# Optimization experiments

Measured on AMD Instinct MI355X. Metric: run time of the kernel, lower is better.

Reference implementation:

```python
import jax, jax.numpy as jnp
import numpy as np

DIM = 512
HEADS = 8
HEAD = DIM // HEADS
T = 243          # temporal length, fixed by get_temporal_mask(243, ...)
N_JOINTS = 17    # skeleton joints
BATCH = 4        # number of clips; leading dim of x is BATCH*T
WINDOWS = (9, 27, 81, 243)  # temporal_MoE_type


def _temporal_masks():
    # Block-diagonal window masks: 0 inside each window block, -100000 outside,
    # exactly matching get_temporal_mask + torch.where(matrix == 0, -100000, 0).
    idx = np.arange(T)
    masks = np.stack([
        np.where((idx[:, None] // w) == (idx[None, :] // w), 0.0, -100000.0)
        for w in WINDOWS
    ]).astype(np.float32)  # (E, T, T)
    return jnp.asarray(masks)


def setup_inputs() -> dict:
    key = jax.random.key(0)
    k0, k1, k2, k3 = jax.random.split(key, 4)
    scaled = lambda k, shape, fan: jax.random.normal(k, shape, jnp.float32) * (fan ** -0.5)
    return {
        "x": jax.random.normal(k0, (BATCH * T, N_JOINTS, DIM), jnp.float32),
        "qkv_w": scaled(k1, (DIM, 3 * DIM), DIM),          # qkv (no bias, qkv_bias=False)
        "proj_w": scaled(k2, (DIM, DIM), DIM),             # output projection
        "proj_b": jnp.zeros((DIM,), jnp.float32),
        "te_w": scaled(k3, (DIM, len(WINDOWS)), DIM),      # temporal_expert_linear
        "te_b": jnp.zeros((len(WINDOWS),), jnp.float32),
        "seqlen": T,
    }


def reference(x, qkv_w, proj_w, proj_b, te_w, te_b, seqlen):
    BT, n, C = x.shape              # (b*T, N, C)
    b = BT // seqlen
    scale = HEAD ** -0.5
    # qkv projection -> q,k,v each (b, H, N, T, head_dim)
    qkv = (x @ qkv_w).reshape(b, seqlen, n, 3, HEADS, HEAD)
    qkv = jnp.transpose(qkv, (3, 0, 4, 2, 1, 5))  # (3, b, H, N, T, c)
    q, k, v = qkv[0], qkv[1], qkv[2]
    # temporal attention logits, shared across experts: (b, H, N, T, T)
    attn = jnp.einsum('bhntc,bhnsc->bhnts', q, k) * scale
    masks = _temporal_masks()                       # (E, T, T)
    attn = attn[None] + masks[:, None, None, None]  # (E, b, H, N, T, T)
    attn = jax.nn.softmax(attn, axis=-1)            # attn_drop is identity (p=0 / eval)
    eo = jnp.einsum('ebhnts,bhnsc->ebhntc', attn, v)
    E = masks.shape[0]
    # (E,b,H,N,T,c) -> (E,b,T,N,H,c) -> (E, b*T, N, C), matching permute(0,3,2,1,4)
    eo = jnp.transpose(eo, (0, 1, 4, 3, 2, 5)).reshape(E, BT, n, C)
    # expert gating: softmax(temporal_expert_linear(x)) over experts, per token
    w = jax.nn.softmax(x @ te_w + te_b, axis=-1)    # (BT, N, E)
    out = jnp.einsum('ebnc,bne->bnc', eo, w)        # fused expert recombination
    out = out @ proj_w + proj_b                     # proj (proj_drop identity)
    return out
```

## Files before the change

kernel.cpp:

```cpp
#include <hip/hip_runtime.h>
#include <hip/hip_bf16.h>
#include <cstdint>

#define TT 243
#define NJ 17
#define NB 4
#define NH 8
#define HD 64
#define CDIM 512
#define NROWS (NB*TT*NJ)
#define NBHN (NB*NH*NJ)

typedef unsigned short u16;
typedef __attribute__((ext_vector_type(8))) short short8;
typedef __attribute__((ext_vector_type(4))) float f32x4;

#define MFMA16(a, b, c) __builtin_amdgcn_mfma_f32_16x16x32_bf16((a), (b), (c), 0, 0, 0)

__device__ __forceinline__ void gl_lds16(const void* g, void* l) {
  __builtin_amdgcn_global_load_lds(
      (const __attribute__((address_space(1))) void*)g,
      (__attribute__((address_space(3))) void*)l, 16, 0, 0);
}

__device__ __forceinline__ u16 f2bf(float f) {
  union { float f; unsigned u; } v; v.f = f;
  unsigned r = v.u + 0x7FFFu + ((v.u >> 16) & 1u);
  return (u16)(r >> 16);
}

__device__ __forceinline__ float wave_reduce_sum(float v) {
#pragma unroll
  for (int off = 32; off > 0; off >>= 1) v += __shfl_xor(v, off, 64);
  return v;
}

__global__ __launch_bounds__(256) void convgates(
    const float* __restrict__ x, const float* __restrict__ te_w,
    const float* __restrict__ te_b, u16* __restrict__ xb,
    float* __restrict__ gates) {
  int w = threadIdx.x >> 6, l = threadIdx.x & 63;
  int row = blockIdx.x * 4 + w;
  if (row >= NROWS) return;
  const float* xr = x + (size_t)row * CDIM;
  u16* xo = xb + (size_t)row * CDIM;
  float a0 = 0.f, a1 = 0.f, a2 = 0.f, a3 = 0.f;
#pragma unroll
  for (int p = 0; p < 2; ++p) {
    int c = (p * 64 + l) * 4;
    float4 v = *(const float4*)(xr + c);
    ushort4 o;
    o.x = f2bf(v.x); o.y = f2bf(v.y); o.z = f2bf(v.z); o.w = f2bf(v.w);
    *(ushort4*)(xo + c) = o;
    float xv[4] = {v.x, v.y, v.z, v.w};
#pragma unroll
    for (int q = 0; q < 4; ++q) {
      float4 wv = *(const float4*)(te_w + (size_t)(c + q) * 4);
      a0 += xv[q] * wv.x; a1 += xv[q] * wv.y;
      a2 += xv[q] * wv.z; a3 += xv[q] * wv.w;
    }
  }
  a0 = wave_reduce_sum(a0);
  a1 = wave_reduce_sum(a1);
  a2 = wave_reduce_sum(a2);
  a3 = wave_reduce_sum(a3);
  a0 += te_b[0]; a1 += te_b[1]; a2 += te_b[2]; a3 += te_b[3];
  float mx = fmaxf(fmaxf(a0, a1), fmaxf(a2, a3));
  float e0 = __expf(a0 - mx), e1 = __expf(a1 - mx);
  float e2 = __expf(a2 - mx), e3 = __expf(a3 - mx);
  float inv = 1.f / (e0 + e1 + e2 + e3);
  if (l == 0) {
    *(float4*)(gates + (size_t)row * 4) =
        make_float4(e0 * inv, e1 * inv, e2 * inv, e3 * inv);
  }
}

__global__ __launch_bounds__(256) void trans_w(const float* __restrict__ in,
                                               u16* __restrict__ out, int K, int N) {
  __shared__ float tile[32][33];
  int n0 = blockIdx.x * 32, k0 = blockIdx.y * 32;
  int tx = threadIdx.x & 31, ty = threadIdx.x >> 5;
#pragma unroll
  for (int p = 0; p < 4; ++p)
    tile[ty + p * 8][tx] = in[(size_t)(k0 + ty + p * 8) * N + n0 + tx];
  __syncthreads();
#pragma unroll
  for (int p = 0; p < 4; ++p)
    out[(size_t)(n0 + ty + p * 8) * K + k0 + tx] = f2bf(tile[tx][ty + p * 8]);
}

__global__ __launch_bounds__(256) void qkv_gemm(
    const u16* __restrict__ xb, const u16* __restrict__ wt,
    u16* __restrict__ qh, u16* __restrict__ kh, u16* __restrict__ vb) {
  __shared__ u16 S[16640];
  u16* Al = S;
  u16* Bl = S + 8192;
  int tid = threadIdx.x;
  int w = tid >> 6, l = tid & 63;
  int c16 = tid & 15, g4 = (tid >> 4) & 3;
  int r0 = blockIdx.x * 128, n0 = blockIdx.y * 128;
  int wm = w & 1, wn = w >> 1;

  size_t arow[2]; int ac8[2], brow[2];
#pragma unroll
  for (int it = 0; it < 2; ++it) {
    int F = it * 256 + w * 64 + l;
    int row = F >> 2;
    ac8[it] = F & 3;
    brow[it] = n0 + row;
    int m = r0 + row; if (m >= NROWS) m = NROWS - 1;
    int bj = m / 243, t = m - bj * 243;
    int b = bj / 17, j = bj - b * 17;
    arow[it] = ((size_t)(b * 243 + t) * 17 + j) * 512;
  }

  f32x4 acc[4][4] = {};
  for (int k0 = 0; k0 < CDIM; k0 += 32) {
    __syncthreads();
#pragma unroll
    for (int it = 0; it < 2; ++it) {
      gl_lds16(xb + arow[it] + k0 + ac8[it] * 8,
               Al + (size_t)(it * 256 + w * 64) * 8);
      gl_lds16(wt + (size_t)brow[it] * 512 + k0 + ac8[it] * 8,
               Bl + (size_t)(it * 256 + w * 64) * 8);
    }
    __syncthreads();
    short8 af[4], bf[4];
#pragma unroll
    for (int i = 0; i < 4; ++i)
      af[i] = *(const short8*)(Al + ((wm * 64 + i * 16 + c16) * 32 + g4 * 8));
#pragma unroll
    for (int j = 0; j < 4; ++j)
      bf[j] = *(const short8*)(Bl + ((wn * 64 + j * 16 + c16) * 32 + g4 * 8));
#pragma unroll
    for (int i = 0; i < 4; ++i)
#pragma unroll
      for (int j = 0; j < 4; ++j)
        acc[i][j] = MFMA16(af[i], bf[j], acc[i][j]);
  }

  if (n0 < 1024) {
#pragma unroll
    for (int i = 0; i < 4; ++i)
#pragma unroll
      for (int r = 0; r < 4; ++r) {
        int m = r0 + wm * 64 + i * 16 + g4 * 4 + r;
        if (m >= NROWS) continue;
        int bj = m / 243, t = m - bj * 243;
        int b = bj / 17, j = bj - b * 17;
#pragma unroll
        for (int jt = 0; jt < 4; ++jt) {
          int col = n0 + wn * 64 + jt * 16 + c16;
          int sel = col >> 9, h = (col >> 6) & 7, c = col & 63;
          u16* dst = sel ? kh : qh;
          dst[((size_t)((b * 8 + h) * 17 + j) * 243 + t) * 64 + c] =
              f2bf(acc[i][jt][r]);
        }
      }
  } else {
    __syncthreads();
#pragma unroll
    for (int i = 0; i < 4; ++i)
#pragma unroll
      for (int jt = 0; jt < 4; ++jt)
#pragma unroll
        for (int r = 0; r < 4; ++r) {
          int row = wm * 64 + i * 16 + g4 * 4 + r;
          int colI = wn * 64 + jt * 16 + c16;
          S[colI * 130 + row] = f2bf(acc[i][jt][r]);
        }
    __syncthreads();
    int hb = (n0 - 1024) >> 6;
    int m0 = r0 + 2 * l;
    int m1 = m0 + 1;
    bool v0 = m0 < NROWS, v1 = m1 < NROWS;
    int bj0 = m0 / 243, t0 = m0 - bj0 * 243;
    int b0 = bj0 / 17, j0 = bj0 - b0 * 17;
    int bj1 = m1 / 243, t1 = m1 - bj1 * 243;
    int b1 = bj1 / 17, j1 = bj1 - b1 * 17;
    size_t base0 = ((size_t)(b0 * 136 + j0) * 64) * 256 + t0;
    size_t base1 = ((size_t)(b1 * 136 + j1) * 64) * 256 + t1;
#pragma unroll 8
    for (int cc = 0; cc < 32; ++cc) {
      int colI = w * 32 + cc;
      int h = hb + (colI >> 6), c = colI & 63;
      ushort2 u = *(const ushort2*)&S[colI * 130 + 2 * l];
      size_t hoff = ((size_t)h * 17 * 64) * 256 + (size_t)c * 256;
      if (v0) vb[base0 + hoff] = u.x;
      if (v1) vb[base1 + hoff] = u.y;
    }
  }
}

__global__ __launch_bounds__(256) void attn_kernel(
    const u16* __restrict__ qh, const u16* __restrict__ kh,
    const u16* __restrict__ vb, const float* __restrict__ gates,
    u16* __restrict__ preb) {
  __shared__ u16 L[32768];
  int bhn = blockIdx.x;
  int q0 = blockIdx.y * 64;
  int b = bhn / (NH * NJ);
  int hj = bhn - b * (NH * NJ);
  int h = hj / NJ, j = hj - (hj / NJ) * NJ;
  int tid = threadIdx.x;
  int w = tid >> 6, l = tid & 63;
  int c16 = tid & 15, g4 = (tid >> 4) & 3;
  int qw = w * 16;

#pragma unroll
  for (int it = 0; it < 8; ++it) {
    int F = it * 256 + w * 64 + l;
    int s = F >> 3;
    int c8 = (F & 7) ^ (s & 7);
    int sg = s < TT ? s : TT - 1;
    gl_lds16(kh + ((size_t)bhn * 243 + sg) * 64 + c8 * 8,
             L + (size_t)(it * 256 + w * 64) * 8);
  }
#pragma unroll
  for (int it = 0; it < 2; ++it) {
    int F = it * 256 + w * 64 + l;
    int q = F >> 3;
    int c8 = (F & 7) ^ (q & 7);
    int t = q0 + q; int tg = t < TT ? t : TT - 1;
    gl_lds16(qh + ((size_t)bhn * 243 + tg) * 64 + c8 * 8,
             L + 16384 + (size_t)(it * 256 + w * 64) * 8);
  }
  __syncthreads();

  short8 aq[2];
#pragma unroll
  for (int hh = 0; hh < 2; ++hh) {
    int q = qw + c16;
    aq[hh] = *(const short8*)(L + 16384 + q * 64 + ((hh * 4 + g4) ^ (q & 7)) * 8);
  }
  f32x4 acc[16];
#pragma unroll
  for (int st = 0; st < 16; ++st) acc[st] = (f32x4)(0.f);
#pragma unroll
  for (int st = 0; st < 16; ++st) {
    int s = st * 16 + c16;
#pragma unroll
    for (int hh = 0; hh < 2; ++hh) {
      short8 bk = *(const short8*)(L + s * 64 + ((hh * 4 + g4) ^ (s & 7)) * 8);
      acc[st] = MFMA16(aq[hh], bk, acc[st]);
    }
  }
  __syncthreads();

#pragma unroll
  for (int it = 0; it < 8; ++it) {
    int F = it * 256 + w * 64 + l;
    int c = F >> 5;
    int slot = F & 31;
    int c8 = (slot & 24) | ((slot & 7) ^ (c & 7));
    gl_lds16(vb + ((size_t)bhn * 64 + c) * 256 + c8 * 8,
             L + 16384 + (size_t)(it * 256 + w * 64) * 8);
  }

  int tr[4], t9[4], t27[4], t81[4];
#pragma unroll
  for (int r = 0; r < 4; ++r) {
    tr[r] = q0 + qw + g4 * 4 + r;
    t9[r] = tr[r] / 9; t27[r] = t9[r] / 3; t81[r] = t27[r] / 3;
  }
#pragma unroll
  for (int st = 0; st < 16; ++st) {
    int s = st * 16 + c16;
#pragma unroll
    for (int r = 0; r < 4; ++r) {
      float v = acc[st][r] * 0.125f;
      acc[st][r] = (s < TT) ? v : -1e30f;
    }
  }
  float M[4];
#pragma unroll
  for (int r = 0; r < 4; ++r) {
    float m = -1e30f;
#pragma unroll
    for (int st = 0; st < 16; ++st) m = fmaxf(m, acc[st][r]);
    m = fmaxf(m, __shfl_xor(m, 1, 64));
    m = fmaxf(m, __shfl_xor(m, 2, 64));
    m = fmaxf(m, __shfl_xor(m, 4, 64));
    m = fmaxf(m, __shfl_xor(m, 8, 64));
    M[r] = m;
  }
#pragma unroll
  for (int st = 0; st < 16; ++st)
#pragma unroll
    for (int r = 0; r < 4; ++r) acc[st][r] = __expf(acc[st][r] - M[r]);
  int s9[16], s27[16], s81[16];
#pragma unroll
  for (int st = 0; st < 16; ++st) {
    int s = st * 16 + c16;
    s9[st] = s / 9; s27[st] = s9[st] / 3; s81[st] = s27[st] / 3;
  }
  float l9[4], l27[4], l81[4], l243[4];
#pragma unroll
  for (int r = 0; r < 4; ++r) { l9[r] = 0.f; l27[r] = 0.f; l81[r] = 0.f; l243[r] = 0.f; }
#pragma unroll
  for (int st = 0; st < 16; ++st)
#pragma unroll
    for (int r = 0; r < 4; ++r) {
      float e = acc[st][r];
      l243[r] += e;
      l9[r]  += (s9[st]  == t9[r])  ? e : 0.f;
      l27[r] += (s27[st] == t27[r]) ? e : 0.f;
      l81[r] += (s81[st] == t81[r]) ? e : 0.f;
    }
#pragma unroll
  for (int r = 0; r < 4; ++r) {
#pragma unroll
    for (int d = 1; d <= 8; d <<= 1) {
      l9[r]   += __shfl_xor(l9[r], d, 64);
      l27[r]  += __shfl_xor(l27[r], d, 64);
      l81[r]  += __shfl_xor(l81[r], d, 64);
      l243[r] += __shfl_xor(l243[r], d, 64);
    }
  }
  float c0[4], c1[4], c2[4], c3[4];
#pragma unroll
  for (int r = 0; r < 4; ++r) {
    int tg = tr[r] < TT ? tr[r] : TT - 1;
    float4 g = *(const float4*)(gates + ((size_t)(b * TT + tg) * NJ + j) * 4);
    c0[r] = g.x / l9[r]; c1[r] = g.y / l27[r];
    c2[r] = g.z / l81[r]; c3[r] = g.w / l243[r];
  }
#pragma unroll
  for (int st = 0; st < 16; ++st) {
    int s = st * 16 + c16;
#pragma unroll
    for (int r = 0; r < 4; ++r) {
      float cw = c3[r];
      cw += (s81[st] == t81[r]) ? c2[r] : 0.f;
      cw += (s27[st] == t27[r]) ? c1[r] : 0.f;
      cw += (s9[st]  == t9[r])  ? c0[r] : 0.f;
      float rv = acc[st][r] * cw;
      if (tr[r] >= TT || s >= TT) rv = 0.f;
      int q = qw + g4 * 4 + r;
      int s8 = s >> 3;
      int slot = (s8 & 24) | ((s8 & 7) ^ (q & 7));
      L[q * 256 + slot * 8 + (s & 7)] = f2bf(rv);
    }
  }
  __syncthreads();

  short8 ar[8];
#pragma unroll
  for (int h2 = 0; h2 < 8; ++h2) {
    int q = qw + c16;
    int c8 = h2 * 4 + g4;
    int slot = (c8 & 24) | ((c8 & 7) ^ (q & 7));
    ar[h2] = *(const short8*)(L + q * 256 + slot * 8);
  }
  f32x4 o[4];
#pragma unroll
  for (int jt = 0; jt < 4; ++jt) o[jt] = (f32x4)(0.f);
#pragma unroll
  for (int jt = 0; jt < 4; ++jt) {
    int c = jt * 16 + c16;
#pragma unroll
    for (int h2 = 0; h2 < 8; ++h2) {
      int c8 = h2 * 4 + g4;
      int slot = (c8 & 24) | ((c8 & 7) ^ (c & 7));
      short8 bv = *(const short8*)(L + 16384 + c * 256 + slot * 8);
      o[jt] = MFMA16(ar[h2], bv, o[jt]);
    }
  }
#pragma unroll
  for (int jt = 0; jt < 4; ++jt)
#pragma unroll
    for (int r = 0; r < 4; ++r) {
      int t = tr[r];
      if (t < TT)
        preb[((size_t)(b * TT + t) * NJ + j) * 512 + h * 64 + jt * 16 + c16] =
            f2bf(o[jt][r]);
    }
}

__global__ __launch_bounds__(256) void proj_gemm(
    const u16* __restrict__ preb, const u16* __restrict__ pwt,
    const float* __restrict__ bias, float* __restrict__ out) {
  __shared__ u16 Al[128 * 32];
  __shared__ u16 Bl[128 * 32];
  int tid = threadIdx.x;
  int w = tid >> 6, l = tid & 63;
  int c16 = tid & 15, g4 = (tid >> 4) & 3;
  int r0 = blockIdx.x * 128, n0 = blockIdx.y * 128;
  int wm = w & 1, wn = w >> 1;
  f32x4 acc[4][4] = {};
  for (int k0 = 0; k0 < CDIM; k0 += 32) {
    __syncthreads();
#pragma unroll
    for (int it = 0; it < 2; ++it) {
      int F = it * 256 + w * 64 + l;
      int row = F >> 2, c8 = F & 3;
      int gr = r0 + row; gr = gr < NROWS ? gr : NROWS - 1;
      gl_lds16(preb + (size_t)gr * 512 + k0 + c8 * 8,
               Al + (size_t)(it * 256 + w * 64) * 8);
      gl_lds16(pwt + (size_t)(n0 + row) * 512 + k0 + c8 * 8,
               Bl + (size_t)(it * 256 + w * 64) * 8);
    }
    __syncthreads();
    short8 af[4], bf[4];
#pragma unroll
    for (int i = 0; i < 4; ++i)
      af[i] = *(const short8*)(Al + ((wm * 64 + i * 16 + c16) * 32 + g4 * 8));
#pragma unroll
    for (int j = 0; j < 4; ++j)
      bf[j] = *(const short8*)(Bl + ((wn * 64 + j * 16 + c16) * 32 + g4 * 8));
#pragma unroll
    for (int i = 0; i < 4; ++i)
#pragma unroll
      for (int j = 0; j < 4; ++j)
        acc[i][j] = MFMA16(af[i], bf[j], acc[i][j]);
  }
#pragma unroll
  for (int i = 0; i < 4; ++i)
#pragma unroll
    for (int r = 0; r < 4; ++r) {
      int row = r0 + wm * 64 + i * 16 + g4 * 4 + r;
      if (row >= NROWS) continue;
#pragma unroll
      for (int jt = 0; jt < 4; ++jt) {
        int col = n0 + wn * 64 + jt * 16 + c16;
        out[(size_t)row * 512 + col] = acc[i][jt][r] + bias[col];
      }
    }
}

extern "C" void kernel_launch(void* const* d_in, const int* in_sizes, int n_in,
                              void* d_out, int out_size, void* d_ws, size_t ws_size,
                              hipStream_t stream) {
  (void)in_sizes; (void)n_in; (void)out_size; (void)ws_size;
  const float* x      = (const float*)d_in[0];
  const float* qkv_w  = (const float*)d_in[1];
  const float* proj_w = (const float*)d_in[2];
  const float* proj_b = (const float*)d_in[3];
  const float* te_w   = (const float*)d_in[4];
  const float* te_b   = (const float*)d_in[5];

  char* p = (char*)d_ws;
  auto alloc = [&](size_t bytes) {
    void* r = (void*)p;
    p += (bytes + 255) & ~(size_t)255;
    return r;
  };
  u16*   xb    = (u16*)alloc((size_t)NROWS * 512 * 2);
  u16*   wt    = (u16*)alloc((size_t)1536 * 512 * 2);
  u16*   pwt   = (u16*)alloc((size_t)512 * 512 * 2);
  float* gates = (float*)alloc((size_t)NROWS * 4 * 4);
  u16*   qhb   = (u16*)alloc((size_t)NBHN * 243 * 64 * 2);
  u16*   khb   = (u16*)alloc((size_t)NBHN * 243 * 64 * 2);
  u16*   vb    = (u16*)alloc((size_t)NBHN * 64 * 256 * 2);
  u16*   preb  = (u16*)alloc((size_t)NROWS * 512 * 2);
  float* out   = (float*)d_out;

  hipLaunchKernelGGL(convgates, dim3((NROWS + 3) / 4), dim3(256), 0, stream,
                     x, te_w, te_b, xb, gates);
  hipLaunchKernelGGL(trans_w, dim3(48, 16), dim3(256), 0, stream,
                     qkv_w, wt, 512, 1536);
  hipLaunchKernelGGL(trans_w, dim3(16, 16), dim3(256), 0, stream,
                     proj_w, pwt, 512, 512);
  hipLaunchKernelGGL(qkv_gemm, dim3((NROWS + 127) / 128, 12), dim3(256), 0, stream,
                     xb, wt, qhb, khb, vb);
  hipLaunchKernelGGL(attn_kernel, dim3(NBHN, 4), dim3(256), 0, stream,
                     qhb, khb, vb, gates, preb);
  hipLaunchKernelGGL(proj_gemm, dim3((NROWS + 127) / 128, 4), dim3(256), 0, stream,
                     preb, pwt, proj_b, out);
}
```

Before: 241.9 us.

## Process all query tiles per head-joint block, reusing LDS-resident K

The attention kernel now launches one block per (batch, head, joint) instead of four. Each block loads K into LDS once and loops over the four 64-row query tiles, so K is no longer reloaded per tile. Q and V fragments are read straight from global memory rather than staged through LDS. The probability tile goes into a per-wave LDS scratch area, which removes most block-wide barriers. The trade-off is a quarter as many blocks, so less parallelism to hide latency, and more global-load latency inside the MFMA loops.

```diff
diff --git a/kernel.cpp b/kernel.cpp
--- a/kernel.cpp
+++ b/kernel.cpp
@@ -197,184 +197,161 @@
     const u16* __restrict__ vb, const float* __restrict__ gates,
     u16* __restrict__ preb) {
   __shared__ u16 L[32768];
+  const int Rb = 15552;
   int bhn = blockIdx.x;
-  int q0 = blockIdx.y * 64;
   int b = bhn / (NH * NJ);
   int hj = bhn - b * (NH * NJ);
-  int h = hj / NJ, j = hj - (hj / NJ) * NJ;
+  int h = hj / NJ, j = hj - h * NJ;
   int tid = threadIdx.x;
-  int w = tid >> 6, l = tid & 63;
+  int w = tid >> 6;
   int c16 = tid & 15, g4 = (tid >> 4) & 3;
-  int qw = w * 16;
+  const u16* Kp = kh + (size_t)bhn * (TT * HD);
+  const u16* Qp = qh + (size_t)bhn * (TT * HD);
+  const u16* Vp = vb + (size_t)bhn * (HD * 256);
+  u16* Rw = L + Rb + w * 4096;
 
 #pragma unroll
   for (int it = 0; it < 8; ++it) {
-    int F = it * 256 + w * 64 + l;
-    int s = F >> 3;
-    int c8 = (F & 7) ^ (s & 7);
-    int sg = s < TT ? s : TT - 1;
-    gl_lds16(kh + ((size_t)bhn * 243 + sg) * 64 + c8 * 8,
-             L + (size_t)(it * 256 + w * 64) * 8);
-  }
-#pragma unroll
-  for (int it = 0; it < 2; ++it) {
-    int F = it * 256 + w * 64 + l;
-    int q = F >> 3;
-    int c8 = (F & 7) ^ (q & 7);
-    int t = q0 + q; int tg = t < TT ? t : TT - 1;
-    gl_lds16(qh + ((size_t)bhn * 243 + tg) * 64 + c8 * 8,
-             L + 16384 + (size_t)(it * 256 + w * 64) * 8);
+    int F = it * 256 + tid;
+    if (F < 1944) {
+      int s = F >> 3;
+      int c8 = (F & 7) ^ (s & 7);
+      gl_lds16(Kp + (size_t)s * 64 + c8 * 8, L + (size_t)(it * 256 + (tid & ~63)) * 8);
+    }
   }
   __syncthreads();
 
-  short8 aq[2];
-#pragma unroll
-  for (int hh = 0; hh < 2; ++hh) {
-    int q = qw + c16;
-    aq[hh] = *(const short8*)(L + 16384 + q * 64 + ((hh * 4 + g4) ^ (q & 7)) * 8);
-  }
-  f32x4 acc[16];
-#pragma unroll
-  for (int st = 0; st < 16; ++st) acc[st] = (f32x4)(0.f);
-#pragma unroll
-  for (int st = 0; st < 16; ++st) {
-    int s = st * 16 + c16;
-#pragma unroll
-    for (int hh = 0; hh < 2; ++hh) {
-      short8 bk = *(const short8*)(L + s * 64 + ((hh * 4 + g4) ^ (s & 7)) * 8);
-      acc[st] = MFMA16(aq[hh], bk, acc[st]);
-    }
-  }
-  __syncthreads();
-
-#pragma unroll
-  for (int it = 0; it < 8; ++it) {
-    int F = it * 256 + w * 64 + l;
-    int c = F >> 5;
-    int slot = F & 31;
-    int c8 = (slot & 24) | ((slot & 7) ^ (c & 7));
-    gl_lds16(vb + ((size_t)bhn * 64 + c) * 256 + c8 * 8,
-             L + 16384 + (size_t)(it * 256 + w * 64) * 8);
-  }
-
-  int tr[4], t9[4], t27[4], t81[4];
-#pragma unroll
-  for (int r = 0; r < 4; ++r) {
-    tr[r] = q0 + qw + g4 * 4 + r;
-    t9[r] = tr[r] / 9; t27[r] = t9[r] / 3; t81[r] = t27[r] / 3;
-  }
-#pragma unroll
-  for (int st = 0; st < 16; ++st) {
-    int s = st * 16 + c16;
+  for (int qt = 0; qt < 4; ++qt) {
+    int qw = qt * 64 + w * 16;
+
+    short8 aq[2];
+#pragma unroll
+    for (int hh = 0; hh < 2; ++hh)
+      aq[hh] = *(const short8*)(Qp + (size_t)(qw + c16) * 64 + hh * 32 + g4 * 8);
+
+    f32x4 acc[16];
+#pragma unroll
+    for (int st = 0; st < 16; ++st) acc[st] = (f32x4)(0.f);
+#pragma unroll
+    for (int st = 0; st < 16; ++st) {
+      int s = st * 16 + c16;
+#pragma unroll
+      for (int hh = 0; hh < 2; ++hh) {
+        short8 bk = *(const short8*)(L + s * 64 + ((hh * 4 + g4) ^ (s & 7)) * 8);
+        acc[st] = MFMA16(aq[hh], bk, acc[st]);
+      }
+    }
+
+    int tr[4], t9[4], t27[4], t81[4];
 #pragma unroll
     for (int r = 0; r < 4; ++r) {
-      float v = acc[st][r] * 0.125f;
-      acc[st][r] = (s < TT) ? v : -1e30f;
-    }
-  }
-  float M[4];
-#pragma unroll
-  for (int r = 0; r < 4; ++r) {
-    float m = -1e30f;
-#pragma unroll
-    for (int st = 0; st < 16; ++st) m = fmaxf(m, acc[st][r]);
-    m = fmaxf(m, __shfl_xor(m, 1, 64));
-    m = fmaxf(m, __shfl_xor(m, 2, 64));
-    m = fmaxf(m, __shfl_xor(m, 4, 64));
-    m = fmaxf(m, __shfl_xor(m, 8, 64));
-    M[r] = m;
-  }
-#pragma unroll
-  for (int st = 0; st < 16; ++st)
-#pragma unroll
-    for (int r = 0; r < 4; ++r) acc[st][r] = __expf(acc[st][r] - M[r]);
-  int s9[16], s27[16], s81[16];
-#pragma unroll
-  for (int st = 0; st < 16; ++st) {
-    int s = st * 16 + c16;
-    s9[st] = s / 9; s27[st] = s9[st] / 3; s81[st] = s27[st] / 3;
-  }
-  float l9[4], l27[4], l81[4], l243[4];
-#pragma unroll
-  for (int r = 0; r < 4; ++r) { l9[r] = 0.f; l27[r] = 0.f; l81[r] = 0.f; l243[r] = 0.f; }
-#pragma unroll
-  for (int st = 0; st < 16; ++st)
+      tr[r] = qw + g4 * 4 + r;
+      t9[r] = tr[r] / 9; t27[r] = t9[r] / 3; t81[r] = t27[r] / 3;
+    }
+#pragma unroll
+    for (int st = 0; st < 16; ++st) {
+      int s = st * 16 + c16;
+#pragma unroll
+      for (int r = 0; r < 4; ++r) {
+        float v = acc[st][r] * 0.125f;
+        acc[st][r] = (s < TT) ? v : -1e30f;
+      }
+    }
+    float M[4];
 #pragma unroll
     for (int r = 0; r < 4; ++r) {
-      float e = acc[st][r];
-      l243[r] += e;
-      l9[r]  += (s9[st]  == t9[r])  ? e : 0.f;
-      l27[r] += (s27[st] == t27[r]) ? e : 0.f;
-      l81[r] += (s81[st] == t81[r]) ? e : 0.f;
-    }
-#pragma unroll
-  for (int r = 0; r < 4; ++r) {
-#pragma unroll
-    for (int d = 1; d <= 8; d <<= 1) {
-      l9[r]   += __shfl_xor(l9[r], d, 64);
-      l27[r]  += __shfl_xor(l27[r], d, 64);
-      l81[r]  += __shfl_xor(l81[r], d, 64);
-      l243[r] += __shfl_xor(l243[r], d, 64);
-    }
-  }
-  float c0[4], c1[4], c2[4], c3[4];
-#pragma unroll
-  for (int r = 0; r < 4; ++r) {
-    int tg = tr[r] < TT ? tr[r] : TT - 1;
-    float4 g = *(const float4*)(gates + ((size_t)(b * TT + tg) * NJ + j) * 4);
-    c0[r] = g.x / l9[r]; c1[r] = g.y / l27[r];
-    c2[r] = g.z / l81[r]; c3[r] = g.w / l243[r];
-  }
-#pragma unroll
-  for (int st = 0; st < 16; ++st) {
-    int s = st * 16 + c16;
+      float m = -1e30f;
+#pragma unroll
+      for (int st = 0; st < 16; ++st) m = fmaxf(m, acc[st][r]);
+      m = fmaxf(m, __shfl_xor(m, 1, 64));
+      m = fmaxf(m, __shfl_xor(m, 2, 64));
+      m = fmaxf(m, __shfl_xor(m, 4, 64));
+      m = fmaxf(m, __shfl_xor(m, 8, 64));
+      M[r] = m;
+    }
+#pragma unroll
+    for (int st = 0; st < 16; ++st)
+#pragma unroll
+      for (int r = 0; r < 4; ++r) acc[st][r] = __expf(acc[st][r] - M[r]);
+    int s9[16], s27[16], s81[16];
+#pragma unroll
+    for (int st = 0; st < 16; ++st) {
+      int s = st * 16 + c16;
+      s9[st] = s / 9; s27[st] = s9[st] / 3; s81[st] = s27[st] / 3;
+    }
+    float l9[4], l27[4], l81[4], l243[4];
+#pragma unroll
+    for (int r = 0; r < 4; ++r) { l9[r] = 0.f; l27[r] = 0.f; l81[r] = 0.f; l243[r] = 0.f; }
+#pragma unroll
+    for (int st = 0; st < 16; ++st)
+#pragma unroll
+      for (int r = 0; r < 4; ++r) {
+        float e = acc[st][r];
+        l243[r] += e;
+        l9[r]  += (s9[st]  == t9[r])  ? e : 0.f;
+        l27[r] += (s27[st] == t27[r]) ? e : 0.f;
+        l81[r] += (s81[st] == t81[r]) ? e : 0.f;
+      }
 #pragma unroll
     for (int r = 0; r < 4; ++r) {
-      float cw = c3[r];
-      cw += (s81[st] == t81[r]) ? c2[r] : 0.f;
-      cw += (s27[st] == t27[r]) ? c1[r] : 0.f;
-      cw += (s9[st]  == t9[r])  ? c0[r] : 0.f;
-      float rv = acc[st][r] * cw;
-      if (tr[r] >= TT || s >= TT) rv = 0.f;
-      int q = qw + g4 * 4 + r;
-      int s8 = s >> 3;
-      int slot = (s8 & 24) | ((s8 & 7) ^ (q & 7));
-      L[q * 256 + slot * 8 + (s & 7)] = f2bf(rv);
-    }
-  }
-  __syncthreads();
-
-  short8 ar[8];
-#pragma unroll
-  for (int h2 = 0; h2 < 8; ++h2) {
-    int q = qw + c16;
-    int c8 = h2 * 4 + g4;
-    int slot = (c8 & 24) | ((c8 & 7) ^ (q & 7));
-    ar[h2] = *(const short8*)(L + q * 256 + slot * 8);
-  }
-  f32x4 o[4];
-#pragma unroll
-  for (int jt = 0; jt < 4; ++jt) o[jt] = (f32x4)(0.f);
-#pragma unroll
-  for (int jt = 0; jt < 4; ++jt) {
-    int c = jt * 16 + c16;
+#pragma unroll
+      for (int d = 1; d <= 8; d <<= 1) {
+        l9[r]   += __shfl_xor(l9[r], d, 64);
+        l27[r]  += __shfl_xor(l27[r], d, 64);
+        l81[r]  += __shfl_xor(l81[r], d, 64);
+        l243[r] += __shfl_xor(l243[r], d, 64);
+      }
+    }
+    float c0[4], c1[4], c2[4], c3[4];
+#pragma unroll
+    for (int r = 0; r < 4; ++r) {
+      int tg = tr[r] < TT ? tr[r] : TT - 1;
+      float4 g = *(const float4*)(gates + ((size_t)(b * TT + tg) * NJ + j) * 4);
+      c0[r] = g.x / l9[r]; c1[r] = g.y / l27[r];
+      c2[r] = g.z / l81[r]; c3[r] = g.w / l243[r];
+    }
+#pragma unroll
+    for (int st = 0; st < 16; ++st) {
+      int s = st * 16 + c16;
+#pragma unroll
+      for (int r = 0; r < 4; ++r) {
+        float cw = c3[r];
+        cw += (s81[st] == t81[r]) ? c2[r] : 0.f;
+        cw += (s27[st] == t27[r]) ? c1[r] : 0.f;
+        cw += (s9[st]  == t9[r])  ? c0[r] : 0.f;
+        float rv = acc[st][r] * cw;
+        if (tr[r] >= TT || s >= TT) rv = 0.f;
+        int q = g4 * 4 + r;
+        int s8 = s >> 3;
+        int slot = (s8 & 24) | ((s8 & 7) ^ (q & 7));
+        Rw[q * 256 + slot * 8 + (s & 7)] = f2bf(rv);
+      }
+    }
+
+    short8 ar[8];
 #pragma unroll
     for (int h2 = 0; h2 < 8; ++h2) {
-      int c8 = h2 * 4 + g4;
-      int slot = (c8 & 24) | ((c8 & 7) ^ (c & 7));
-      short8 bv = *(const short8*)(L + 16384 + c * 256 + slot * 8);
-      o[jt] = MFMA16(ar[h2], bv, o[jt]);
-    }
-  }
-#pragma unroll
-  for (int jt = 0; jt < 4; ++jt)
-#pragma unroll
-    for (int r = 0; r < 4; ++r) {
-      int t = tr[r];
-      if (t < TT)
-        preb[((size_t)(b * TT + t) * NJ + j) * 512 + h * 64 + jt * 16 + c16] =
-            f2bf(o[jt][r]);
-    }
+      int cc = h2 * 4 + g4;
+      int slot = (cc & 24) | ((cc & 7) ^ (c16 & 7));
+      ar[h2] = *(const short8*)(Rw + c16 * 256 + slot * 8);
+    }
+#pragma unroll
+    for (int jt = 0; jt < 4; ++jt) {
+      int c = jt * 16 + c16;
+      f32x4 o = (f32x4)(0.f);
+#pragma unroll
+      for (int h2 = 0; h2 < 8; ++h2) {
+        short8 bv = *(const short8*)(Vp + (size_t)c * 256 + h2 * 32 + g4 * 8);
+        o = MFMA16(ar[h2], bv, o);
+      }
+#pragma unroll
+      for (int r = 0; r < 4; ++r) {
+        int t = tr[r];
+        if (t < TT)
+          preb[((size_t)(b * TT + t) * NJ + j) * 512 + h * 64 + c] = f2bf(o[r]);
+      }
+    }
+  }
 }
 
 __global__ __launch_bounds__(256) void proj_gemm(
@@ -463,7 +440,7 @@
                      proj_w, pwt, 512, 512);
   hipLaunchKernelGGL(qkv_gemm, dim3((NROWS + 127) / 128, 12), dim3(256), 0, stream,
                      xb, wt, qhb, khb, vb);
-  hipLaunchKernelGGL(attn_kernel, dim3(NBHN, 4), dim3(256), 0, stream,
+  hipLaunchKernelGGL(attn_kernel, dim3(NBHN), dim3(256), 0, stream,
                      qhb, khb, vb, gates, preb);
   hipLaunchKernelGGL(proj_gemm, dim3((NROWS + 127) / 128, 4), dim3(256), 0, stream,
                      preb, pwt, proj_b, out);
```

Result: slower. 297.0 us (+22.8%).
